# Kernel tuning notes

Measured on AMD Instinct MI355X. Metric: run time of the kernel, lower is better.

## Reference

```python
import jax, jax.numpy as jnp
import numpy as np

N = 50000      # nodes
E = 800000     # edges (before self-loops)
IN = 128       # in_channels
HID = 64       # hidden_channels
HEADS = 4
OUT = 64       # out_channels
SLOPE = 0.2    # negative_slope


def setup_inputs() -> dict:
    key = jax.random.key(0)
    ks = jax.random.split(key, 16)

    def p(k, shape, fan_in):
        return jax.random.normal(k, shape, dtype=jnp.float32) / np.float32(np.sqrt(fan_in))

    inp = jax.random.normal(ks[0], (N, IN), dtype=jnp.float32)
    edge_index = jax.random.randint(ks[1], (2, E), 0, N, dtype=jnp.int32)

    W1 = p(ks[2], (IN, HEADS * HID), IN)
    att_src1 = p(ks[3], (1, HEADS, HID), HID)
    att_dst1 = p(ks[4], (1, HEADS, HID), HID)
    b1 = jnp.zeros((HEADS * HID,), jnp.float32)

    W2 = p(ks[5], (HEADS * HID, HEADS * HID), HEADS * HID)
    att_src2 = p(ks[6], (1, HEADS, HID), HID)
    att_dst2 = p(ks[7], (1, HEADS, HID), HID)
    b2 = jnp.zeros((HEADS * HID,), jnp.float32)

    W3 = p(ks[8], (HEADS * HID, HEADS * OUT), HEADS * HID)
    att_src3 = p(ks[9], (1, HEADS, OUT), OUT)
    att_dst3 = p(ks[10], (1, HEADS, OUT), OUT)
    b3 = jnp.zeros((HEADS * OUT,), jnp.float32)

    return dict(inp=inp, edge_index=edge_index,
                W1=W1, att_src1=att_src1, att_dst1=att_dst1, b1=b1,
                W2=W2, att_src2=att_src2, att_dst2=att_dst2, b2=b2,
                W3=W3, att_src3=att_src3, att_dst3=att_dst3, b3=b3)


def _gat_conv(x, W, a_src, a_dst, b, src, dst, H, C):
    """One PyG-style GATConv (concat=True, dropout=0, self-loops already in src/dst)."""
    n = x.shape[0]
    h = (x @ W).reshape(n, H, C)                     # [N,H,C]
    alpha_src = jnp.sum(h * a_src, axis=-1)          # [N,H]
    alpha_dst = jnp.sum(h * a_dst, axis=-1)          # [N,H]
    e = jax.nn.leaky_relu(alpha_src[src] + alpha_dst[dst], SLOPE)  # [Etot,H]
    # segment softmax over incoming edges of each destination node
    emax = jax.ops.segment_max(e, dst, num_segments=n)             # [N,H]
    ee = jnp.exp(e - emax[dst])
    denom = jax.ops.segment_sum(ee, dst, num_segments=n)           # [N,H]
    alpha = ee / denom[dst]                                        # [Etot,H]
    out = jax.ops.segment_sum(alpha[:, :, None] * h[src], dst, num_segments=n)  # [N,H,C]
    return out.reshape(n, H * C) + b


def reference(inp, edge_index, W1, att_src1, att_dst1, b1,
              W2, att_src2, att_dst2, b2, W3, att_src3, att_dst3, b3):
    n = inp.shape[0]
    loops = jnp.arange(n, dtype=edge_index.dtype)
    src = jnp.concatenate([edge_index[0], loops])  # add self-loops (PyG default)
    dst = jnp.concatenate([edge_index[1], loops])
    h1 = jax.nn.elu(_gat_conv(inp, W1, att_src1, att_dst1, b1, src, dst, HEADS, HID))
    h2 = jax.nn.elu(_gat_conv(h1, W2, att_src2, att_dst2, b2, src, dst, HEADS, HID))
    oup = jax.nn.elu(_gat_conv(h2, W3, att_src3, att_dst3, b3, src, dst, HEADS, OUT))
    return oup
```

## Files before the change

### kernel.cpp

```cpp
#include <hip/hip_runtime.h>
#include <hip/hip_bf16.h>
#include <stdint.h>

#define HEADS 4
#define SLOPE 0.2f

typedef unsigned short u16;
typedef float f32x4 __attribute__((ext_vector_type(4)));
typedef short s16x8 __attribute__((ext_vector_type(8)));
typedef unsigned short u16x4 __attribute__((ext_vector_type(4)));

__device__ __forceinline__ u16 f2bf(float f) {
    unsigned int u = __float_as_uint(f);
    u = (u + 0x7fffu + ((u >> 16) & 1u)) >> 16;
    return (u16)u;
}
__device__ __forceinline__ float bf2f(u16 v) {
    return __uint_as_float(((unsigned int)v) << 16);
}
__device__ __forceinline__ float fin(float x) {
    return (x == x && fabsf(x) < 1e30f) ? x : 0.f;
}

__global__ void prep_kernel(const float* __restrict__ inp, u16* __restrict__ Xb,
                            const float* __restrict__ W1, u16* __restrict__ Wt1,
                            const float* __restrict__ W2, u16* __restrict__ Wt2,
                            const float* __restrict__ W3, u16* __restrict__ Wt3,
                            const int* __restrict__ dst, int* __restrict__ deg,
                            int* __restrict__ rank, int E, int N) {
    int i = blockIdx.x * blockDim.x + threadIdx.x;
    int Etot = E + N;
    if (i < Etot) {
        int d = (i < E) ? dst[i] : (i - E);
        d = ((unsigned)d < (unsigned)N) ? d : 0;
        rank[i] = atomicAdd(&deg[d], 1);
        return;
    }
    i -= Etot;
    int cast4 = N * 32;
    if (i < cast4) {
        f32x4 v = *(const f32x4*)(inp + (size_t)i * 4);
        u16x4 o;
        #pragma unroll
        for (int j = 0; j < 4; j++) o[j] = f2bf(fin(v[j]));
        *(u16x4*)(Xb + (size_t)i * 4) = o;
        return;
    }
    i -= cast4;
    if (i >= 0 && i < 128 * 256) {
        int k = i >> 8, m = i & 255;
        Wt1[m * 128 + k] = f2bf(fin(W1[i]));
        return;
    }
    i -= 128 * 256;
    if (i >= 0 && i < 256 * 256) {
        int k = i >> 8, m = i & 255;
        Wt2[m * 256 + k] = f2bf(fin(W2[i]));
        return;
    }
    i -= 256 * 256;
    if (i >= 0 && i < 256 * 256) {
        int k = i >> 8, m = i & 255;
        Wt3[m * 256 + k] = f2bf(fin(W3[i]));
    }
}

__global__ __launch_bounds__(256) void scan_kernel(const int* __restrict__ deg,
                                                   int* __restrict__ rowstart, int N) {
    __shared__ int wsum[4];
    __shared__ int sm[256];
    int b = blockIdx.x, tid = threadIdx.x;
    int start = b * 1024;
    int pre = 0;
    for (int i = tid; i < start; i += 256) pre += deg[i];
    #pragma unroll
    for (int off = 1; off <= 32; off <<= 1) pre += __shfl_xor(pre, off);
    if ((tid & 63) == 0) wsum[tid >> 6] = pre;
    __syncthreads();
    int block_pre = wsum[0] + wsum[1] + wsum[2] + wsum[3];

    int base = start + tid * 4;
    int v[4]; int s = 0;
    #pragma unroll
    for (int j = 0; j < 4; j++) { int i = base + j; v[j] = (i < N) ? deg[i] : 0; s += v[j]; }
    sm[tid] = s;
    __syncthreads();
    for (int off = 1; off < 256; off <<= 1) {
        int t = (tid >= off) ? sm[tid - off] : 0;
        __syncthreads();
        sm[tid] += t;
        __syncthreads();
    }
    int run = block_pre + sm[tid] - s;
    #pragma unroll
    for (int j = 0; j < 4; j++) {
        int i = base + j;
        if (i < N) { rowstart[i] = run; run += v[j]; }
    }
    if (b == gridDim.x - 1 && tid == 255) rowstart[N] = block_pre + sm[255];
}

__global__ void place_kernel(const int* __restrict__ src, const int* __restrict__ dst,
                             const int* __restrict__ rowstart, const int* __restrict__ rank,
                             int* __restrict__ csr, int E, int N) {
    int i = blockIdx.x * blockDim.x + threadIdx.x;
    if (i < E + N) {
        int s, d;
        if (i < E) { s = src[i]; d = dst[i]; }
        else       { s = i - E; d = i - E; }
        s = ((unsigned)s < (unsigned)N) ? s : 0;
        d = ((unsigned)d < (unsigned)N) ? d : 0;
        int pos = rowstart[d] + rank[i];
        if ((unsigned)pos < (unsigned)(E + N)) csr[pos] = s;
    }
}

__global__ __launch_bounds__(256, 3) void gemm_kernel(
        const u16* __restrict__ X, const u16* __restrict__ Wt,
        u16* __restrict__ Hout, const float* __restrict__ att_src,
        const float* __restrict__ att_dst, float* __restrict__ as_out,
        float* __restrict__ ad_out, int N, int K) {
    __shared__ __align__(16) u16 As[64 * 72];
    __shared__ __align__(16) u16 Bs[256 * 72];
    int t = threadIdx.x;
    int wv = t >> 6, lane = t & 63;
    int quad = lane >> 4, l16 = lane & 15;
    int m0 = blockIdx.x * 64;
    int n0 = wv * 64;
    int srow = t >> 3, sslot = t & 7;

    f32x4 acc[4][4];
    #pragma unroll
    for (int r = 0; r < 4; r++)
        #pragma unroll
        for (int c = 0; c < 4; c++) acc[r][c] = (f32x4){0.f, 0.f, 0.f, 0.f};

    const int nsteps = K >> 6;
    s16x8 ra[2], rb[8];
    {
        #pragma unroll
        for (int s = 0; s < 2; s++) {
            int rg = m0 + s * 32 + srow; rg = rg < N ? rg : N - 1;
            ra[s] = *(const s16x8*)(X + (size_t)rg * K + sslot * 8);
        }
        #pragma unroll
        for (int s = 0; s < 8; s++) {
            int n = s * 32 + srow;
            rb[s] = *(const s16x8*)(Wt + (size_t)n * K + sslot * 8);
        }
    }
    for (int step = 0; step < nsteps; step++) {
        __syncthreads();
        #pragma unroll
        for (int s = 0; s < 2; s++)
            *(s16x8*)(As + (s * 32 + srow) * 72 + sslot * 8) = ra[s];
        #pragma unroll
        for (int s = 0; s < 8; s++)
            *(s16x8*)(Bs + (s * 32 + srow) * 72 + sslot * 8) = rb[s];
        __syncthreads();
        if (step + 1 < nsteps) {
            int k0 = (step + 1) << 6;
            #pragma unroll
            for (int s = 0; s < 2; s++) {
                int rg = m0 + s * 32 + srow; rg = rg < N ? rg : N - 1;
                ra[s] = *(const s16x8*)(X + (size_t)rg * K + k0 + sslot * 8);
            }
            #pragma unroll
            for (int s = 0; s < 8; s++) {
                int n = s * 32 + srow;
                rb[s] = *(const s16x8*)(Wt + (size_t)n * K + k0 + sslot * 8);
            }
        }
        #pragma unroll
        for (int subk = 0; subk < 2; subk++) {
            s16x8 af[4], bfr[4];
            #pragma unroll
            for (int r = 0; r < 4; r++)
                af[r] = *(const s16x8*)(As + (r * 16 + l16) * 72 + subk * 32 + quad * 8);
            #pragma unroll
            for (int c = 0; c < 4; c++)
                bfr[c] = *(const s16x8*)(Bs + (n0 + c * 16 + l16) * 72 + subk * 32 + quad * 8);
            #pragma unroll
            for (int r = 0; r < 4; r++)
                #pragma unroll
                for (int c = 0; c < 4; c++)
                    acc[r][c] = __builtin_amdgcn_mfma_f32_16x16x32_bf16(af[r], bfr[c], acc[r][c], 0, 0, 0);
        }
    }

    float aps[4][4], apd[4][4];
    #pragma unroll
    for (int r = 0; r < 4; r++)
        #pragma unroll
        for (int j = 0; j < 4; j++) { aps[r][j] = 0.f; apd[r][j] = 0.f; }

    #pragma unroll
    for (int r = 0; r < 4; r++) {
        int rowb = m0 + r * 16 + quad * 4;
        #pragma unroll
        for (int c = 0; c < 4; c++) {
            int col = n0 + c * 16 + l16;
            float av = fin(att_src[col]);
            float dv = fin(att_dst[col]);
            #pragma unroll
            for (int j = 0; j < 4; j++) {
                int row = rowb + j;
                float v = acc[r][c][j];
                aps[r][j] += v * av;
                apd[r][j] += v * dv;
                if (row < N) Hout[(size_t)row * 256 + col] = f2bf(v);
            }
        }
    }
    #pragma unroll
    for (int off = 1; off <= 8; off <<= 1)
        #pragma unroll
        for (int r = 0; r < 4; r++)
            #pragma unroll
            for (int j = 0; j < 4; j++) {
                aps[r][j] += __shfl_xor(aps[r][j], off);
                apd[r][j] += __shfl_xor(apd[r][j], off);
            }
    if (l16 == 0) {
        #pragma unroll
        for (int r = 0; r < 4; r++) {
            int rowb = m0 + r * 16 + quad * 4;
            #pragma unroll
            for (int j = 0; j < 4; j++) {
                int row = rowb + j;
                if (row < N) {
                    as_out[row * 4 + wv] = aps[r][j];
                    ad_out[row * 4 + wv] = apd[r][j];
                }
            }
        }
    }
}

__global__ __launch_bounds__(256) void gather_kernel(
        const u16* __restrict__ Hb, const float* __restrict__ asrc,
        const float* __restrict__ adst, const int* __restrict__ rowstart,
        const int* __restrict__ csr, const float* __restrict__ bias,
        u16* __restrict__ outb, float* __restrict__ outf, int write_f32,
        int N, int Etot) {
    int wv = threadIdx.x >> 6, lane = threadIdx.x & 63;
    int n = blockIdx.x * 4 + wv;
    if (n >= N) return;
    int es = lane >> 5, c = lane & 31;
    int h = c >> 3;
    int i0 = rowstart[n], i1 = rowstart[n + 1];
    i0 = min(max(i0, 0), Etot);
    i1 = min(max(i1, i0), Etot);

    float adh = adst[n * 4 + h];
    float acc[8];
    float ws = 0.f;
    #pragma unroll
    for (int j = 0; j < 8; j++) acc[j] = 0.f;

    int i = i0 + es;
    for (; i + 6 < i1; i += 8) {
        int ss[4];
        #pragma unroll
        for (int u = 0; u < 4; u++) {
            int s = csr[i + 2 * u];
            ss[u] = ((unsigned)s < (unsigned)N) ? s : 0;
        }
        float e[4]; s16x8 hv[4];
        #pragma unroll
        for (int u = 0; u < 4; u++) {
            e[u] = asrc[ss[u] * 4 + h] + adh;
            hv[u] = *(const s16x8*)(Hb + (size_t)ss[u] * 256 + c * 8);
        }
        #pragma unroll
        for (int u = 0; u < 4; u++) {
            float ee = e[u] > 0.f ? e[u] : SLOPE * e[u];
            float w = __expf(fminf(ee, 80.f));
            ws += w;
            #pragma unroll
            for (int j = 0; j < 8; j++) acc[j] += w * bf2f((u16)hv[u][j]);
        }
    }
    for (; i + 2 < i1; i += 4) {
        int sA = csr[i], sB = csr[i + 2];
        sA = ((unsigned)sA < (unsigned)N) ? sA : 0;
        sB = ((unsigned)sB < (unsigned)N) ? sB : 0;
        float eA = asrc[sA * 4 + h] + adh;
        float eB = asrc[sB * 4 + h] + adh;
        s16x8 hvA = *(const s16x8*)(Hb + (size_t)sA * 256 + c * 8);
        s16x8 hvB = *(const s16x8*)(Hb + (size_t)sB * 256 + c * 8);
        eA = eA > 0.f ? eA : SLOPE * eA;
        eB = eB > 0.f ? eB : SLOPE * eB;
        float wA = __expf(fminf(eA, 80.f));
        float wB = __expf(fminf(eB, 80.f));
        ws += wA + wB;
        #pragma unroll
        for (int j = 0; j < 8; j++)
            acc[j] += wA * bf2f((u16)hvA[j]) + wB * bf2f((u16)hvB[j]);
    }
    if (i < i1) {
        int s = csr[i];
        s = ((unsigned)s < (unsigned)N) ? s : 0;
        float e = asrc[s * 4 + h] + adh;
        s16x8 hv = *(const s16x8*)(Hb + (size_t)s * 256 + c * 8);
        e = e > 0.f ? e : SLOPE * e;
        float w = __expf(fminf(e, 80.f));
        ws += w;
        #pragma unroll
        for (int j = 0; j < 8; j++) acc[j] += w * bf2f((u16)hv[j]);
    }

    ws += __shfl_xor(ws, 32);
    #pragma unroll
    for (int j = 0; j < 8; j++) acc[j] += __shfl_xor(acc[j], 32);

    if (es == 0) {
        float invh = (ws > 0.f) ? 1.f / ws : 0.f;
        f32x4 blo = *(const f32x4*)(bias + c * 8);
        f32x4 bhi = *(const f32x4*)(bias + c * 8 + 4);
        size_t base = (size_t)n * 256 + c * 8;
        float o[8];
        #pragma unroll
        for (int j = 0; j < 8; j++) {
            float v = acc[j] * invh + fin(j < 4 ? blo[j] : bhi[j - 4]);
            o[j] = v > 0.f ? v : (__expf(v) - 1.f);
        }
        if (write_f32) {
            f32x4 lo = {o[0], o[1], o[2], o[3]}, hi = {o[4], o[5], o[6], o[7]};
            *(f32x4*)(outf + base) = lo;
            *(f32x4*)(outf + base + 4) = hi;
        } else {
            s16x8 ob;
            #pragma unroll
            for (int j = 0; j < 8; j++) ob[j] = (short)f2bf(o[j]);
            *(s16x8*)(outb + base) = ob;
        }
    }
}

extern "C" void kernel_launch(void* const* d_in, const int* in_sizes, int n_in,
                              void* d_out, int out_size, void* d_ws, size_t ws_size,
                              hipStream_t stream) {
    const float* inp  = (const float*)d_in[0];
    const int*   ei   = (const int*)d_in[1];
    const float* W1   = (const float*)d_in[2];
    const float* at_s1= (const float*)d_in[3];
    const float* at_d1= (const float*)d_in[4];
    const float* b1   = (const float*)d_in[5];
    const float* W2   = (const float*)d_in[6];
    const float* at_s2= (const float*)d_in[7];
    const float* at_d2= (const float*)d_in[8];
    const float* b2   = (const float*)d_in[9];
    const float* W3   = (const float*)d_in[10];
    const float* at_s3= (const float*)d_in[11];
    const float* at_d3= (const float*)d_in[12];
    const float* b3   = (const float*)d_in[13];

    const int N = in_sizes[0] / 128;
    const int E = in_sizes[1] / 2;
    const int Etot = E + N;
    const int* esrc = ei;
    const int* edst = ei + E;

    char* p = (char*)d_ws;
    auto alloc = [&](size_t b) -> void* {
        void* q = (void*)p;
        p += (b + 255) & ~(size_t)255;
        return q;
    };
    u16*   Xb       = (u16*)alloc((size_t)N * 256 * 2);
    u16*   Hb       = (u16*)alloc((size_t)N * 256 * 2);
    u16*   Wt1      = (u16*)alloc((size_t)128 * 256 * 2);
    u16*   Wt2      = (u16*)alloc((size_t)256 * 256 * 2);
    u16*   Wt3      = (u16*)alloc((size_t)256 * 256 * 2);
    float* asb      = (float*)alloc((size_t)N * 4 * 4);
    float* adb      = (float*)alloc((size_t)N * 4 * 4);
    int*   deg      = (int*)alloc((size_t)N * 4);
    int*   rowstart = (int*)alloc((size_t)(N + 1) * 4);
    int*   rank     = (int*)alloc((size_t)Etot * 4);
    int*   csr      = (int*)alloc((size_t)Etot * 4);
    float* outf     = (float*)d_out;

    const int SB = (N + 1023) / 1024;
    const int prep_total = Etot + N * 32 + 128 * 256 + 2 * 256 * 256;

    hipMemsetAsync(deg, 0, (size_t)N * 4, stream);
    prep_kernel<<<(prep_total + 255) / 256, 256, 0, stream>>>(
        inp, Xb, W1, Wt1, W2, Wt2, W3, Wt3, edst, deg, rank, E, N);
    scan_kernel<<<SB, 256, 0, stream>>>(deg, rowstart, N);
    place_kernel<<<(Etot + 255) / 256, 256, 0, stream>>>(esrc, edst, rowstart, rank, csr, E, N);

    const int gemm_grid = (N + 63) / 64;
    const int node_grid = (N + 3) / 4;

    gemm_kernel<<<gemm_grid, 256, 0, stream>>>(Xb, Wt1, Hb, at_s1, at_d1, asb, adb, N, 128);
    gather_kernel<<<node_grid, 256, 0, stream>>>(Hb, asb, adb, rowstart, csr, b1,
                                                 Xb, outf, 0, N, Etot);
    gemm_kernel<<<gemm_grid, 256, 0, stream>>>(Xb, Wt2, Hb, at_s2, at_d2, asb, adb, N, 256);
    gather_kernel<<<node_grid, 256, 0, stream>>>(Hb, asb, adb, rowstart, csr, b2,
                                                 Xb, outf, 0, N, Etot);
    gemm_kernel<<<gemm_grid, 256, 0, stream>>>(Xb, Wt3, Hb, at_s3, at_d3, asb, adb, N, 256);
    gather_kernel<<<node_grid, 256, 0, stream>>>(Hb, asb, adb, rowstart, csr, b3,
                                                 Xb, outf, 1, N, Etot);
}
```

Measured before the change: 445.4 us.

## Pad degree counters, tile weight transpose via LDS, nontemporal CSR stores

```diff
diff --git a/kernel.cpp b/kernel.cpp
--- a/kernel.cpp
+++ b/kernel.cpp
@@ -4,6 +4,7 @@
 
 #define HEADS 4
 #define SLOPE 0.2f
+#define DEGS 16
 
 typedef unsigned short u16;
 typedef float f32x4 __attribute__((ext_vector_type(4)));
@@ -28,40 +29,55 @@
                             const float* __restrict__ W3, u16* __restrict__ Wt3,
                             const int* __restrict__ dst, int* __restrict__ deg,
                             int* __restrict__ rank, int E, int N) {
-    int i = blockIdx.x * blockDim.x + threadIdx.x;
+    __shared__ u16 tile[64][68];
     int Etot = E + N;
-    if (i < Etot) {
-        int d = (i < E) ? dst[i] : (i - E);
-        d = ((unsigned)d < (unsigned)N) ? d : 0;
-        rank[i] = atomicAdd(&deg[d], 1);
+    int CB = (Etot + 255) >> 8;
+    int XB = (N * 32 + 255) >> 8;
+    int b = blockIdx.x;
+    if (b < CB) {
+        int i = b * 256 + threadIdx.x;
+        if (i < Etot) {
+            int d = (i < E) ? dst[i] : (i - E);
+            d = ((unsigned)d < (unsigned)N) ? d : 0;
+            rank[i] = atomicAdd(&deg[d * DEGS], 1);
+        }
         return;
     }
-    i -= Etot;
-    int cast4 = N * 32;
-    if (i < cast4) {
-        f32x4 v = *(const f32x4*)(inp + (size_t)i * 4);
+    b -= CB;
+    if (b < XB) {
+        int i = b * 256 + threadIdx.x;
+        if (i < N * 32) {
+            f32x4 v = *(const f32x4*)(inp + (size_t)i * 4);
+            u16x4 o;
+            #pragma unroll
+            for (int j = 0; j < 4; j++) o[j] = f2bf(fin(v[j]));
+            *(u16x4*)(Xb + (size_t)i * 4) = o;
+        }
+        return;
+    }
+    b -= XB;
+    const float* W; u16* Wt; int K, kt, mt;
+    if (b < 8)       { W = W1; Wt = Wt1; K = 128; kt = b >> 2; mt = b & 3; }
+    else if (b < 24) { b -= 8;  W = W2; Wt = Wt2; K = 256; kt = b >> 2; mt = b & 3; }
+    else             { b -= 24; W = W3; Wt = Wt3; K = 256; kt = b >> 2; mt = b & 3; }
+    int k0 = kt * 64, m0 = mt * 64;
+    int t = threadIdx.x;
+    int rr = t >> 4, cc = (t & 15) * 4;
+    #pragma unroll
+    for (int j = 0; j < 4; j++) {
+        int row = rr + 16 * j;
+        f32x4 v = *(const f32x4*)(W + (size_t)(k0 + row) * 256 + m0 + cc);
+        #pragma unroll
+        for (int q = 0; q < 4; q++) tile[row][cc + q] = f2bf(fin(v[q]));
+    }
+    __syncthreads();
+    #pragma unroll
+    for (int j = 0; j < 4; j++) {
+        int orow = rr + 16 * j;
         u16x4 o;
         #pragma unroll
-        for (int j = 0; j < 4; j++) o[j] = f2bf(fin(v[j]));
-        *(u16x4*)(Xb + (size_t)i * 4) = o;
-        return;
-    }
-    i -= cast4;
-    if (i >= 0 && i < 128 * 256) {
-        int k = i >> 8, m = i & 255;
-        Wt1[m * 128 + k] = f2bf(fin(W1[i]));
-        return;
-    }
-    i -= 128 * 256;
-    if (i >= 0 && i < 256 * 256) {
-        int k = i >> 8, m = i & 255;
-        Wt2[m * 256 + k] = f2bf(fin(W2[i]));
-        return;
-    }
-    i -= 256 * 256;
-    if (i >= 0 && i < 256 * 256) {
-        int k = i >> 8, m = i & 255;
-        Wt3[m * 256 + k] = f2bf(fin(W3[i]));
+        for (int q = 0; q < 4; q++) o[q] = tile[cc + q][orow];
+        *(u16x4*)(Wt + (size_t)(m0 + orow) * K + k0 + cc) = o;
     }
 }
 
@@ -72,7 +88,7 @@
     int b = blockIdx.x, tid = threadIdx.x;
     int start = b * 1024;
     int pre = 0;
-    for (int i = tid; i < start; i += 256) pre += deg[i];
+    for (int i = tid; i < start; i += 256) pre += deg[i * DEGS];
     #pragma unroll
     for (int off = 1; off <= 32; off <<= 1) pre += __shfl_xor(pre, off);
     if ((tid & 63) == 0) wsum[tid >> 6] = pre;
@@ -82,7 +98,11 @@
     int base = start + tid * 4;
     int v[4]; int s = 0;
     #pragma unroll
-    for (int j = 0; j < 4; j++) { int i = base + j; v[j] = (i < N) ? deg[i] : 0; s += v[j]; }
+    for (int j = 0; j < 4; j++) {
+        int i = base + j;
+        v[j] = (i < N) ? deg[i * DEGS] : 0;
+        s += v[j];
+    }
     sm[tid] = s;
     __syncthreads();
     for (int off = 1; off < 256; off <<= 1) {
@@ -111,7 +131,8 @@
         s = ((unsigned)s < (unsigned)N) ? s : 0;
         d = ((unsigned)d < (unsigned)N) ? d : 0;
         int pos = rowstart[d] + rank[i];
-        if ((unsigned)pos < (unsigned)(E + N)) csr[pos] = s;
+        if ((unsigned)pos < (unsigned)(E + N))
+            __builtin_nontemporal_store(s, csr + pos);
     }
 }
 
@@ -375,17 +396,19 @@
     u16*   Wt3      = (u16*)alloc((size_t)256 * 256 * 2);
     float* asb      = (float*)alloc((size_t)N * 4 * 4);
     float* adb      = (float*)alloc((size_t)N * 4 * 4);
-    int*   deg      = (int*)alloc((size_t)N * 4);
+    int*   deg      = (int*)alloc((size_t)N * DEGS * 4);
     int*   rowstart = (int*)alloc((size_t)(N + 1) * 4);
     int*   rank     = (int*)alloc((size_t)Etot * 4);
     int*   csr      = (int*)alloc((size_t)Etot * 4);
     float* outf     = (float*)d_out;
 
     const int SB = (N + 1023) / 1024;
-    const int prep_total = Etot + N * 32 + 128 * 256 + 2 * 256 * 256;
-
-    hipMemsetAsync(deg, 0, (size_t)N * 4, stream);
-    prep_kernel<<<(prep_total + 255) / 256, 256, 0, stream>>>(
+    const int CB = (Etot + 255) >> 8;
+    const int XB = (N * 32 + 255) >> 8;
+    const int prep_blocks = CB + XB + 40;
+
+    hipMemsetAsync(deg, 0, (size_t)N * DEGS * 4, stream);
+    prep_kernel<<<prep_blocks, 256, 0, stream>>>(
         inp, Xb, W1, Wt1, W2, Wt2, W3, Wt3, edst, deg, rank, E, N);
     scan_kernel<<<SB, 256, 0, stream>>>(deg, rowstart, N);
     place_kernel<<<(Etot + 255) / 256, 256, 0, stream>>>(esrc, edst, rowstart, rank, csr, E, N);
```

After: 463.7 us. 1.04x slower.
